# Kernel tuning notes

Measured on AMD Instinct MI355X. Metric: run time of the kernel, lower is better.

The kernel has to match this reference:

```python
import jax, jax.numpy as jnp
import numpy as np

COMMITMENT_COST = 0.25
KLD_SCALE = 1.0


def setup_inputs() -> dict:
    key = jax.random.key(0)
    k1, k2 = jax.random.split(key)
    z = jax.random.normal(k1, (8, 4096, 512), dtype=jnp.float32)
    embed_w = jax.random.normal(k2, (1024, 512), dtype=jnp.float32)
    return {"z": z, "embed_w": embed_w}


def reference(z, embed_w):
    bsz, s, d = z.shape
    flat = z.reshape(-1, d)  # [N, d]
    dist = (
        jnp.sum(flat * flat, axis=1, keepdims=True)
        - 2.0 * flat @ embed_w.T
        + jnp.sum(embed_w * embed_w, axis=1)[None, :]
    )
    ind = jnp.argmin(dist, axis=1).reshape(bsz, s)  # (-dist).max == dist.min
    z_q = embed_w[ind]  # codebook gather [bsz, s, d]
    sg = jax.lax.stop_gradient
    diff = COMMITMENT_COST * ((sg(z_q) - z) ** 2 + (z_q - sg(z)) ** 2)
    diff = diff * KLD_SCALE
    z_q = z + sg(z_q - z)  # straight-through estimator
    return z_q, diff, ind
```

## Files before the change

kernel.cpp:

```cpp
#include <hip/hip_runtime.h>
#include <math.h>


#define D_DIM   512
#define K_CODES 1024
#define N_TOK   32768

#define BM 128
#define BN 128
#define NKT 16

typedef __attribute__((ext_vector_type(8))) short bf16x8;
typedef __attribute__((ext_vector_type(4))) float f32x4;

__device__ __forceinline__ unsigned short bf16_rne(float f) {
    unsigned int u = __float_as_uint(f);
    return (unsigned short)((u + 0x7FFFu + ((u >> 16) & 1u)) >> 16);
}
__device__ __forceinline__ float bf16_to_f32(unsigned short b) {
    return __uint_as_float(((unsigned int)b) << 16);
}

#define GLOAD16(gp, lp)                                                        \
    __builtin_amdgcn_global_load_lds(                                          \
        (const __attribute__((address_space(1))) void*)(gp),                   \
        (__attribute__((address_space(3))) void*)(lp), 16, 0, 0)

__global__ __launch_bounds__(256) void vq_zsplit(const float* __restrict__ z,
                                                 unsigned short* __restrict__ zhi,
                                                 unsigned short* __restrict__ zlo) {
    const int tid = blockIdx.x * 256 + threadIdx.x;
    const float4* z4 = (const float4*)z;
    ushort4* h4 = (ushort4*)zhi;
    ushort4* l4 = (ushort4*)zlo;
#pragma unroll
    for (int g = 0; g < 8; ++g) {
        const size_t i = (size_t)g * 524288 + tid;
        float4 v = z4[i];
        float f[4] = {v.x, v.y, v.z, v.w};
        unsigned short hb[4], lb[4];
#pragma unroll
        for (int j = 0; j < 4; ++j) {
            hb[j] = bf16_rne(f[j]);
            lb[j] = bf16_rne(f[j] - bf16_to_f32(hb[j]));
        }
        h4[i] = make_ushort4(hb[0], hb[1], hb[2], hb[3]);
        l4[i] = make_ushort4(lb[0], lb[1], lb[2], lb[3]);
    }
}

__global__ __launch_bounds__(256) void vq_prep(const float* __restrict__ ew,
                                               unsigned short* __restrict__ ehi,
                                               unsigned short* __restrict__ elo,
                                               float* __restrict__ e2) {
    const int wv = threadIdx.x >> 6, lane = threadIdx.x & 63;
    const int code = blockIdx.x * 4 + wv;
    const float* row = ew + (size_t)code * D_DIM;
    float s = 0.0f;
#pragma unroll
    for (int h = 0; h < 2; ++h) {
        const int c = h * 256 + lane * 4;
        float4 v = *(const float4*)(row + c);
        float f[4] = {v.x, v.y, v.z, v.w};
        unsigned short hb[4], lb[4];
#pragma unroll
        for (int j = 0; j < 4; ++j) {
            s = fmaf(f[j], f[j], s);
            hb[j] = bf16_rne(f[j]);
            lb[j] = bf16_rne(f[j] - bf16_to_f32(hb[j]));
        }
        *(ushort4*)(ehi + (size_t)code * D_DIM + c) = make_ushort4(hb[0], hb[1], hb[2], hb[3]);
        *(ushort4*)(elo + (size_t)code * D_DIM + c) = make_ushort4(lb[0], lb[1], lb[2], lb[3]);
    }
#pragma unroll
    for (int off = 32; off > 0; off >>= 1) s += __shfl_xor(s, off, 64);
    if (lane == 0) e2[code] = s;
}

__global__ __launch_bounds__(256, 2) void vq_gemm(
    const unsigned short* __restrict__ zhi, const unsigned short* __restrict__ zlo,
    const unsigned short* __restrict__ ehi, const unsigned short* __restrict__ elo,
    const float* __restrict__ e2, float* __restrict__ pv, float* __restrict__ pif) {
    __shared__ __align__(16) unsigned short lds[32768];
    const int AHI = 0, ALO = 4096, BHI = 8192, BLO = 12288;

    const int t = threadIdx.x, lane = t & 63, wv = t >> 6;
    const int b  = blockIdx.x;
    const int wg = (b & 7) * 256 + (b >> 3);
    const int mtile = wg >> 3, ntile = wg & 7;
    const int row0 = mtile * BM;
    const int c0g  = ntile * BN;

    const int idx0 = (wv * 2 + 0) * 64 + lane;
    const int idx1 = (wv * 2 + 1) * 64 + lane;
    const int c_0 = idx0 >> 7, r_0 = idx0 & 127;
    const int c_1 = idx1 >> 7, r_1 = idx1 & 127;
    const size_t zo0 = (size_t)(row0 + r_0) * D_DIM + c_0 * 8;
    const size_t zo1 = (size_t)(row0 + r_1) * D_DIM + c_1 * 8;
    const size_t eo0 = (size_t)(c0g + r_0) * D_DIM + c_0 * 8;
    const size_t eo1 = (size_t)(c0g + r_1) * D_DIM + c_1 * 8;
    const int l0 = (wv * 2 + 0) * 512;
    const int l1 = (wv * 2 + 1) * 512;

    const int wr = wv >> 1, wc = wv & 1;
    const int lm = lane & 15, lk = lane >> 4;

    f32x4 acc[4][4];
    const f32x4 zero4 = {0.f, 0.f, 0.f, 0.f};
#pragma unroll
    for (int i = 0; i < 4; ++i)
#pragma unroll
        for (int j = 0; j < 4; ++j) acc[i][j] = zero4;

    auto stage = [&](int kt, int bufo) {
        const int ko = kt * 32;
        GLOAD16(zhi + zo0 + ko, &lds[bufo + AHI + l0]);
        GLOAD16(zhi + zo1 + ko, &lds[bufo + AHI + l1]);
        GLOAD16(zlo + zo0 + ko, &lds[bufo + ALO + l0]);
        GLOAD16(zlo + zo1 + ko, &lds[bufo + ALO + l1]);
        GLOAD16(ehi + eo0 + ko, &lds[bufo + BHI + l0]);
        GLOAD16(ehi + eo1 + ko, &lds[bufo + BHI + l1]);
        GLOAD16(elo + eo0 + ko, &lds[bufo + BLO + l0]);
        GLOAD16(elo + eo1 + ko, &lds[bufo + BLO + l1]);
    };

    stage(0, 0);
    __syncthreads();

    int cur = 0;
    for (int kt = 0; kt < NKT; ++kt) {
        const int bufo = cur * 16384;
        if (kt + 1 < NKT) stage(kt + 1, (cur ^ 1) * 16384);

        bf16x8 ah[4], al[4], bh[4], bl[4];
#pragma unroll
        for (int mi = 0; mi < 4; ++mi) {
            const int s = (lk * 128 + wr * 64 + mi * 16 + lm) * 8;
            ah[mi] = *(const bf16x8*)&lds[bufo + AHI + s];
            al[mi] = *(const bf16x8*)&lds[bufo + ALO + s];
        }
#pragma unroll
        for (int nj = 0; nj < 4; ++nj) {
            const int s = (lk * 128 + wc * 64 + nj * 16 + lm) * 8;
            bh[nj] = *(const bf16x8*)&lds[bufo + BHI + s];
            bl[nj] = *(const bf16x8*)&lds[bufo + BLO + s];
        }
#pragma unroll
        for (int mi = 0; mi < 4; ++mi)
#pragma unroll
            for (int nj = 0; nj < 4; ++nj)
                acc[mi][nj] = __builtin_amdgcn_mfma_f32_16x16x32_bf16(
                    ah[mi], bh[nj], acc[mi][nj], 0, 0, 0);
#pragma unroll
        for (int mi = 0; mi < 4; ++mi)
#pragma unroll
            for (int nj = 0; nj < 4; ++nj)
                acc[mi][nj] = __builtin_amdgcn_mfma_f32_16x16x32_bf16(
                    ah[mi], bl[nj], acc[mi][nj], 0, 0, 0);
#pragma unroll
        for (int mi = 0; mi < 4; ++mi)
#pragma unroll
            for (int nj = 0; nj < 4; ++nj)
                acc[mi][nj] = __builtin_amdgcn_mfma_f32_16x16x32_bf16(
                    al[mi], bh[nj], acc[mi][nj], 0, 0, 0);

        __syncthreads();
        cur ^= 1;
    }

    float best[16], bidx[16];
#pragma unroll
    for (int i = 0; i < 16; ++i) { best[i] = INFINITY; bidx[i] = 0.f; }
#pragma unroll
    for (int nj = 0; nj < 4; ++nj) {
        const int cloc = wc * 64 + nj * 16 + lm;
        const float e2v = e2[c0g + cloc];
#pragma unroll
        for (int mi = 0; mi < 4; ++mi)
#pragma unroll
            for (int r = 0; r < 4; ++r) {
                const float sc = fmaf(-2.0f, acc[mi][nj][r], e2v);
                const int bi = mi * 4 + r;
                if (sc < best[bi]) { best[bi] = sc; bidx[bi] = (float)(c0g + cloc); }
            }
    }
#pragma unroll
    for (int off = 1; off < 16; off <<= 1) {
#pragma unroll
        for (int bi = 0; bi < 16; ++bi) {
            float v2 = __shfl_xor(best[bi], off, 64);
            float i2 = __shfl_xor(bidx[bi], off, 64);
            if (v2 < best[bi] || (v2 == best[bi] && i2 < bidx[bi])) {
                best[bi] = v2; bidx[bi] = i2;
            }
        }
    }
    __syncthreads();
    float* sv = (float*)lds;
    float* si = sv + 256;
    if (lm == 0) {
#pragma unroll
        for (int mi = 0; mi < 4; ++mi)
#pragma unroll
            for (int r = 0; r < 4; ++r) {
                const int rl = wr * 64 + mi * 16 + lk * 4 + r;
                sv[wc * 128 + rl] = best[mi * 4 + r];
                si[wc * 128 + rl] = bidx[mi * 4 + r];
            }
    }
    __syncthreads();
    if (t < 128) {
        float v0 = sv[t], i0 = si[t];
        float v1 = sv[128 + t], i1 = si[128 + t];
        if (v1 < v0 || (v1 == v0 && i1 < i0)) { v0 = v1; i0 = i1; }
        pv [(size_t)ntile * N_TOK + row0 + t] = v0;
        pif[(size_t)ntile * N_TOK + row0 + t] = i0;
    }
}

__global__ __launch_bounds__(256) void vq_out_kernel(
    const float* __restrict__ z, const float* __restrict__ ew,
    const float* __restrict__ pv, const float* __restrict__ pif,
    float* __restrict__ indf, float* __restrict__ zq, float* __restrict__ diff) {
    const int w    = threadIdx.x >> 6;
    const int lane = threadIdx.x & 63;
    const int row  = blockIdx.x * 4 + w;

    float v = INFINITY, ix = 0.f;
    if (lane < 8) {
        v  = pv [(size_t)lane * N_TOK + row];
        ix = pif[(size_t)lane * N_TOK + row];
    }
#pragma unroll
    for (int off = 1; off < 8; off <<= 1) {
        float v2 = __shfl_xor(v, off, 64);
        float i2 = __shfl_xor(ix, off, 64);
        if (v2 < v || (v2 == v && i2 < ix)) { v = v2; ix = i2; }
    }
    const float ixb = __shfl(ix, 0, 64);
    const int c = (int)ixb;
    if (lane == 0) indf[row] = ixb;

    const float4* z4 = (const float4*)&z[(size_t)row * D_DIM];
    const float4* e4 = (const float4*)&ew[(size_t)c * D_DIM];
    float4* q4 = (float4*)&zq[(size_t)row * D_DIM];
    float4* d4 = (float4*)&diff[(size_t)row * D_DIM];

#pragma unroll
    for (int vv = 0; vv < 2; ++vv) {
        const int i = vv * 64 + lane;
        const float4 zv = z4[i];
        const float4 ev = e4[i];
        float4 qv, dv;
        float ax = ev.x - zv.x, ay = ev.y - zv.y, az = ev.z - zv.z, aw = ev.w - zv.w;
        qv.x = zv.x + ax; qv.y = zv.y + ay; qv.z = zv.z + az; qv.w = zv.w + aw;
        dv.x = 0.5f * (ax * ax); dv.y = 0.5f * (ay * ay);
        dv.z = 0.5f * (az * az); dv.w = 0.5f * (aw * aw);
        q4[i] = qv;
        d4[i] = dv;
    }
}

extern "C" void kernel_launch(void* const* d_in, const int* in_sizes, int n_in,
                              void* d_out, int out_size, void* d_ws, size_t ws_size,
                              hipStream_t stream) {
    const float* z  = (const float*)d_in[0];
    const float* ew = (const float*)d_in[1];
    float* out  = (float*)d_out;
    float* zq   = out;
    float* diff = out + (size_t)N_TOK * D_DIM;
    float* indf = out + (size_t)2 * N_TOK * D_DIM;

    char* s0 = (char*)d_out;
    unsigned short* ehi = (unsigned short*)(s0);
    unsigned short* elo = (unsigned short*)(s0 + (1u << 20));
    float* e2  = (float*)(s0 + (2u << 20));
    unsigned short* zhi = (unsigned short*)diff;
    unsigned short* zlo = zhi + (size_t)N_TOK * D_DIM;
    float* pv  = (float*)d_ws;
    float* pif = (float*)d_ws + (size_t)8 * N_TOK;

    hipLaunchKernelGGL(vq_zsplit, dim3(2048),        dim3(256), 0, stream, z, zhi, zlo);
    hipLaunchKernelGGL(vq_prep,   dim3(K_CODES / 4), dim3(256), 0, stream, ew, ehi, elo, e2);
    hipLaunchKernelGGL(vq_gemm,   dim3(2048),        dim3(256), 0, stream,
                       zhi, zlo, ehi, elo, e2, pv, pif);
    hipLaunchKernelGGL(vq_out_kernel, dim3(N_TOK / 4), dim3(256), 0, stream,
                       z, ew, pv, pif, indf, zq, diff);
}
```

Baseline: 209.8 us.

## Load codebook operand directly from global, halve LDS, raise occupancy

The codebook hi/lo tiles are no longer staged through LDS. Each wave reads its B fragments straight from global memory (L2-resident codebook), which halves the LDS footprint and allows launch bounds of 4 workgroups per CU. The loop is restructured with a barrier at the top, sched barriers and s_setprio around the MFMA block, and lo-fragment loads deferred to cut register pressure. The cost is global-load latency sitting on the MFMA critical path for B, and redundant B reads across waves sharing a column block.

```diff
diff --git a/kernel.cpp b/kernel.cpp
--- a/kernel.cpp
+++ b/kernel.cpp
@@ -9,6 +9,7 @@
 #define BM 128
 #define BN 128
 #define NKT 16
+#define BUFU 8192
 
 typedef __attribute__((ext_vector_type(8))) short bf16x8;
 typedef __attribute__((ext_vector_type(4))) float f32x4;
@@ -25,6 +26,8 @@
     __builtin_amdgcn_global_load_lds(                                          \
         (const __attribute__((address_space(1))) void*)(gp),                   \
         (__attribute__((address_space(3))) void*)(lp), 16, 0, 0)
+
+#define SB0 __builtin_amdgcn_sched_barrier(0)
 
 __global__ __launch_bounds__(256) void vq_zsplit(const float* __restrict__ z,
                                                  unsigned short* __restrict__ zhi,
@@ -77,12 +80,12 @@
     if (lane == 0) e2[code] = s;
 }
 
-__global__ __launch_bounds__(256, 2) void vq_gemm(
+__global__ __launch_bounds__(256, 4) void vq_gemm(
     const unsigned short* __restrict__ zhi, const unsigned short* __restrict__ zlo,
     const unsigned short* __restrict__ ehi, const unsigned short* __restrict__ elo,
     const float* __restrict__ e2, float* __restrict__ pv, float* __restrict__ pif) {
-    __shared__ __align__(16) unsigned short lds[32768];
-    const int AHI = 0, ALO = 4096, BHI = 8192, BLO = 12288;
+    __shared__ __align__(16) unsigned short lds[2 * BUFU];
+    const int AHI = 0, ALO = 4096;
 
     const int t = threadIdx.x, lane = t & 63, wv = t >> 6;
     const int b  = blockIdx.x;
@@ -91,20 +94,20 @@
     const int row0 = mtile * BM;
     const int c0g  = ntile * BN;
 
-    const int idx0 = (wv * 2 + 0) * 64 + lane;
-    const int idx1 = (wv * 2 + 1) * 64 + lane;
-    const int c_0 = idx0 >> 7, r_0 = idx0 & 127;
-    const int c_1 = idx1 >> 7, r_1 = idx1 & 127;
+    const int c_0 = t >> 7,        r_0 = t & 127;
+    const int c_1 = 2 + (t >> 7),  r_1 = t & 127;
     const size_t zo0 = (size_t)(row0 + r_0) * D_DIM + c_0 * 8;
     const size_t zo1 = (size_t)(row0 + r_1) * D_DIM + c_1 * 8;
-    const size_t eo0 = (size_t)(c0g + r_0) * D_DIM + c_0 * 8;
-    const size_t eo1 = (size_t)(c0g + r_1) * D_DIM + c_1 * 8;
-    const int l0 = (wv * 2 + 0) * 512;
-    const int l1 = (wv * 2 + 1) * 512;
+    const int sl0 = t * 8;
+    const int sl1 = (256 + t) * 8;
 
     const int wr = wv >> 1, wc = wv & 1;
     const int lm = lane & 15, lk = lane >> 4;
 
+    const size_t bbase = (size_t)(c0g + wc * 64 + lm) * D_DIM + lk * 8;
+    const unsigned short* __restrict__ bh_p = ehi + bbase;
+    const unsigned short* __restrict__ bl_p = elo + bbase;
+
     f32x4 acc[4][4];
     const f32x4 zero4 = {0.f, 0.f, 0.f, 0.f};
 #pragma unroll
@@ -114,58 +117,58 @@
 
     auto stage = [&](int kt, int bufo) {
         const int ko = kt * 32;
-        GLOAD16(zhi + zo0 + ko, &lds[bufo + AHI + l0]);
-        GLOAD16(zhi + zo1 + ko, &lds[bufo + AHI + l1]);
-        GLOAD16(zlo + zo0 + ko, &lds[bufo + ALO + l0]);
-        GLOAD16(zlo + zo1 + ko, &lds[bufo + ALO + l1]);
-        GLOAD16(ehi + eo0 + ko, &lds[bufo + BHI + l0]);
-        GLOAD16(ehi + eo1 + ko, &lds[bufo + BHI + l1]);
-        GLOAD16(elo + eo0 + ko, &lds[bufo + BLO + l0]);
-        GLOAD16(elo + eo1 + ko, &lds[bufo + BLO + l1]);
+        GLOAD16(zhi + zo0 + ko, &lds[bufo + AHI + sl0]);
+        GLOAD16(zhi + zo1 + ko, &lds[bufo + AHI + sl1]);
+        GLOAD16(zlo + zo0 + ko, &lds[bufo + ALO + sl0]);
+        GLOAD16(zlo + zo1 + ko, &lds[bufo + ALO + sl1]);
     };
 
     stage(0, 0);
-    __syncthreads();
-
-    int cur = 0;
     for (int kt = 0; kt < NKT; ++kt) {
-        const int bufo = cur * 16384;
-        if (kt + 1 < NKT) stage(kt + 1, (cur ^ 1) * 16384);
-
-        bf16x8 ah[4], al[4], bh[4], bl[4];
-#pragma unroll
-        for (int mi = 0; mi < 4; ++mi) {
-            const int s = (lk * 128 + wr * 64 + mi * 16 + lm) * 8;
-            ah[mi] = *(const bf16x8*)&lds[bufo + AHI + s];
-            al[mi] = *(const bf16x8*)&lds[bufo + ALO + s];
-        }
-#pragma unroll
-        for (int nj = 0; nj < 4; ++nj) {
-            const int s = (lk * 128 + wc * 64 + nj * 16 + lm) * 8;
-            bh[nj] = *(const bf16x8*)&lds[bufo + BHI + s];
-            bl[nj] = *(const bf16x8*)&lds[bufo + BLO + s];
-        }
+        const int bufo = (kt & 1) * BUFU;
+        __syncthreads();
+        SB0;
+        if (kt + 1 < NKT) stage(kt + 1, bufo ^ BUFU);
+
+        bf16x8 ah[4], bh[4];
+#pragma unroll
+        for (int mi = 0; mi < 4; ++mi)
+            ah[mi] = *(const bf16x8*)&lds[bufo + AHI + (lk * 128 + wr * 64 + mi * 16 + lm) * 8];
+#pragma unroll
+        for (int nj = 0; nj < 4; ++nj)
+            bh[nj] = *(const bf16x8*)(bh_p + nj * (16 * D_DIM) + kt * 32);
+        __builtin_amdgcn_s_setprio(1);
 #pragma unroll
         for (int mi = 0; mi < 4; ++mi)
 #pragma unroll
             for (int nj = 0; nj < 4; ++nj)
                 acc[mi][nj] = __builtin_amdgcn_mfma_f32_16x16x32_bf16(
                     ah[mi], bh[nj], acc[mi][nj], 0, 0, 0);
-#pragma unroll
-        for (int mi = 0; mi < 4; ++mi)
+        {
+            bf16x8 bl[4];
 #pragma unroll
             for (int nj = 0; nj < 4; ++nj)
-                acc[mi][nj] = __builtin_amdgcn_mfma_f32_16x16x32_bf16(
-                    ah[mi], bl[nj], acc[mi][nj], 0, 0, 0);
-#pragma unroll
-        for (int mi = 0; mi < 4; ++mi)
-#pragma unroll
-            for (int nj = 0; nj < 4; ++nj)
-                acc[mi][nj] = __builtin_amdgcn_mfma_f32_16x16x32_bf16(
-                    al[mi], bh[nj], acc[mi][nj], 0, 0, 0);
-
-        __syncthreads();
-        cur ^= 1;
+                bl[nj] = *(const bf16x8*)(bl_p + nj * (16 * D_DIM) + kt * 32);
+#pragma unroll
+            for (int mi = 0; mi < 4; ++mi)
+#pragma unroll
+                for (int nj = 0; nj < 4; ++nj)
+                    acc[mi][nj] = __builtin_amdgcn_mfma_f32_16x16x32_bf16(
+                        ah[mi], bl[nj], acc[mi][nj], 0, 0, 0);
+        }
+        {
+            bf16x8 al[4];
+#pragma unroll
+            for (int mi = 0; mi < 4; ++mi)
+                al[mi] = *(const bf16x8*)&lds[bufo + ALO + (lk * 128 + wr * 64 + mi * 16 + lm) * 8];
+#pragma unroll
+            for (int mi = 0; mi < 4; ++mi)
+#pragma unroll
+                for (int nj = 0; nj < 4; ++nj)
+                    acc[mi][nj] = __builtin_amdgcn_mfma_f32_16x16x32_bf16(
+                        al[mi], bh[nj], acc[mi][nj], 0, 0, 0);
+        }
+        __builtin_amdgcn_s_setprio(0);
     }
 
     float best[16], bidx[16];
```

New measurement: 252.3 us. 1.2x slower.
